# Optimization experiments

Hardware: AMD Instinct MI355X
Metric: run time of the kernel (lower is better)

The kernel has to match this reference:

```python
import jax, jax.numpy as jnp
import numpy as np

D_IN, H, NH = 256, 512, 8
B, T = 8, 1024


def sinusoidal_pe(seq_len, d_model):
    pos = jnp.arange(seq_len, dtype=jnp.float32)[:, None]
    div = jnp.exp(jnp.arange(0, d_model, 2, dtype=jnp.float32) * (-jnp.log(10000.0) / d_model))
    pe = jnp.zeros((seq_len, d_model), jnp.float32)
    pe = pe.at[:, 0::2].set(jnp.sin(pos * div)).at[:, 1::2].set(jnp.cos(pos * div))
    return pe


def layer_norm(x, g, b, eps=1e-5):
    mu = jnp.mean(x, -1, keepdims=True)
    var = jnp.mean((x - mu) ** 2, -1, keepdims=True)
    return (x - mu) * jax.lax.rsqrt(var + eps) * g + b


def lstm_dir(x, wih, whh, bih, bhh):
    # x: [B,T,H]; wih/whh: [4H,H]; gate order i,f,g,o (PyTorch convention)
    Bx = x.shape[0]
    Hh = whh.shape[1]
    xg = jnp.einsum('bth,gh->btg', x, wih) + bih  # precompute input gates [B,T,4H]

    def step(carry, xg_t):
        h, c = carry
        gates = xg_t + h @ whh.T + bhh
        i, f, g, o = jnp.split(gates, 4, axis=-1)
        c = jax.nn.sigmoid(f) * c + jax.nn.sigmoid(i) * jnp.tanh(g)
        h = jax.nn.sigmoid(o) * jnp.tanh(c)
        return (h, c), h

    h0 = jnp.zeros((Bx, Hh), x.dtype)
    _, hs = jax.lax.scan(step, (h0, h0), xg.transpose(1, 0, 2))
    return hs.transpose(1, 0, 2)  # [B,T,H]


def setup_inputs():
    key = jax.random.key(0)
    ks = jax.random.split(key, 30)
    s = 0.02

    def g(k, shape):
        return jax.random.normal(k, shape, jnp.float32) * s

    return {
        'temporal_data': jax.random.normal(ks[0], (B, T, D_IN), jnp.float32),
        'w_in': g(ks[1], (H, D_IN)), 'b_in': jnp.zeros((H,), jnp.float32),
        'wq': g(ks[2], (H, H)), 'bq': jnp.zeros((H,), jnp.float32),
        'wk': g(ks[3], (H, H)), 'bk': jnp.zeros((H,), jnp.float32),
        'wv': g(ks[4], (H, H)), 'bv': jnp.zeros((H,), jnp.float32),
        'wo': g(ks[5], (H, H)), 'bo': jnp.zeros((H,), jnp.float32),
        'g1': jnp.ones((H,), jnp.float32), 'b1': jnp.zeros((H,), jnp.float32),
        'wih_f': g(ks[6], (4 * H, H)), 'whh_f': g(ks[7], (4 * H, H)),
        'bih_f': jnp.zeros((4 * H,), jnp.float32), 'bhh_f': jnp.zeros((4 * H,), jnp.float32),
        'wih_b': g(ks[8], (4 * H, H)), 'whh_b': g(ks[9], (4 * H, H)),
        'bih_b': jnp.zeros((4 * H,), jnp.float32), 'bhh_b': jnp.zeros((4 * H,), jnp.float32),
        'g2': jnp.ones((2 * H,), jnp.float32), 'b2': jnp.zeros((2 * H,), jnp.float32),
        'w_out': g(ks[10], (H, 2 * H)), 'b_out': jnp.zeros((H,), jnp.float32),
    }


def reference(temporal_data, w_in, b_in, wq, bq, wk, bk, wv, bv, wo, bo, g1, b1,
              wih_f, whh_f, bih_f, bhh_f, wih_b, whh_b, bih_b, bhh_b, g2, b2, w_out, b_out):
    x = temporal_data @ w_in.T + b_in                      # [B,T,H]
    Bx, Tx, _ = x.shape
    x = x + sinusoidal_pe(Tx, H)
    residual = x

    hd = H // NH
    q = (x @ wq.T + bq).reshape(Bx, Tx, NH, hd).transpose(0, 2, 1, 3)
    k = (x @ wk.T + bk).reshape(Bx, Tx, NH, hd).transpose(0, 2, 1, 3)
    v = (x @ wv.T + bv).reshape(Bx, Tx, NH, hd).transpose(0, 2, 1, 3)
    scores = jnp.einsum('bhqd,bhkd->bhqk', q, k) * (hd ** -0.5)
    causal = jnp.triu(jnp.ones((Tx, Tx), bool), 1)
    scores = jnp.where(causal, jnp.float32(-1e9), scores)
    attn = jax.nn.softmax(scores, axis=-1)
    o = jnp.einsum('bhqk,bhkd->bhqd', attn, v).transpose(0, 2, 1, 3).reshape(Bx, Tx, H)
    o = o @ wo.T + bo

    x = layer_norm(o + residual, g1, b1)                   # dropout in eval = identity

    h_fwd = lstm_dir(x, wih_f, whh_f, bih_f, bhh_f)
    h_bwd = jnp.flip(lstm_dir(jnp.flip(x, 1), wih_b, whh_b, bih_b, bhh_b), 1)
    lstm_out = jnp.concatenate([h_fwd, h_bwd], axis=-1)    # [B,T,2H]
    lstm_out = layer_norm(lstm_out, g2, b2)

    emb = jnp.mean(lstm_out, axis=1)                       # [B,2H]
    return emb @ w_out.T + b_out                           # [B,H]
```

## Files before the change

### kernel.cpp

```cpp
#include <hip/hip_runtime.h>

typedef unsigned short u16;
typedef unsigned int   u32;
typedef unsigned long long u64;
typedef __attribute__((ext_vector_type(8))) short short8v;
typedef __attribute__((ext_vector_type(4))) float f32x4;
typedef __attribute__((ext_vector_type(4))) unsigned int u32x4;

#define DINL __device__ __forceinline__

DINL u16 f2bf(float f){ union{float f;u32 u;} v{f}; return (u16)((v.u + 0x7fffu + ((v.u>>16)&1u))>>16); }
DINL float bf2f(u16 b){ union{u32 u;float f;} v{(u32)b<<16}; return v.f; }
DINL f32x4 MFMA16(short8v a, short8v b, f32x4 c){ return __builtin_amdgcn_mfma_f32_16x16x32_bf16(a,b,c,0,0,0); }
DINL void gl16(const void* g, void* l){
  __builtin_amdgcn_global_load_lds((const __attribute__((address_space(1))) void*)g,
                                   (__attribute__((address_space(3))) void*)l, 16, 0, 0);
}
DINL float wredd(float v){
#pragma unroll
  for (int m=1;m<64;m<<=1) v += __shfl_xor(v, m);
  return v;
}
DINL float sigm(float x){ return 1.f/(1.f+__expf(-x)); }
DINL float tanh_(float x){ return 2.f/(1.f+__expf(-2.f*x)) - 1.f; }

__global__ __launch_bounds__(256) void zerok(u32* __restrict__ dst){
  size_t i = ((size_t)blockIdx.x*256 + threadIdx.x)*4;
  u32x4 z = {0,0,0,0};
  *(u32x4*)(dst + i) = z;
}

__global__ __launch_bounds__(256) void cvtk(const float* __restrict__ src, u16* __restrict__ dst, int n){
  int i = (blockIdx.x*256 + threadIdx.x)*4;
  float4 v = *(const float4*)(src + i);
  dst[i+0]=f2bf(v.x); dst[i+1]=f2bf(v.y); dst[i+2]=f2bf(v.z); dst[i+3]=f2bf(v.w);
}

template<int EPI>
__global__ __launch_bounds__(256) void gemm128(
    const u16* __restrict__ A, const u16* __restrict__ W,
    const float* __restrict__ bias0, const float* __restrict__ bias1, const float* __restrict__ bias2,
    const u16* __restrict__ resid, u16* __restrict__ out, int M, int N, int K)
{
  __shared__ __align__(16) u16 Al[128*64];
  __shared__ __align__(16) u16 Bl[128*64];
  const int tid = threadIdx.x, lane = tid & 63, w = tid >> 6;
  const int wr = w >> 1, wc = w & 1;
  const int m0 = blockIdx.y * 128, n0 = blockIdx.x * 128;
  f32x4 acc[4][4] = {};
  for (int k0 = 0; k0 < K; k0 += 64) {
#pragma unroll
    for (int j = 0; j < 4; ++j) {
      int idx = (j*4 + w)*64 + lane;
      int r = idx >> 3, c8 = idx & 7;
      gl16(A + (size_t)(m0 + r)*K + k0 + c8*8, (void*)(Al + (size_t)(j*4+w)*512));
      gl16(W + (size_t)(n0 + r)*K + k0 + c8*8, (void*)(Bl + (size_t)(j*4+w)*512));
    }
    __syncthreads();
#pragma unroll
    for (int kk = 0; kk < 2; ++kk) {
      short8v af[4], bf[4];
#pragma unroll
      for (int i = 0; i < 4; ++i)
        af[i] = *(const short8v*)(Al + ((wr*64 + i*16 + (lane&15))*64 + kk*32 + (lane>>4)*8));
#pragma unroll
      for (int i = 0; i < 4; ++i)
        bf[i] = *(const short8v*)(Bl + ((wc*64 + i*16 + (lane&15))*64 + kk*32 + (lane>>4)*8));
#pragma unroll
      for (int mi=0;mi<4;++mi)
#pragma unroll
        for (int ni=0;ni<4;++ni)
          acc[mi][ni] = MFMA16(af[mi], bf[ni], acc[mi][ni]);
    }
    __syncthreads();
  }
#pragma unroll
  for (int mi=0;mi<4;++mi)
#pragma unroll
    for (int ni=0;ni<4;++ni)
#pragma unroll
      for (int r=0;r<4;++r) {
        int m = m0 + wr*64 + mi*16 + (lane>>4)*4 + r;
        int n = n0 + wc*64 + ni*16 + (lane&15);
        float v = acc[mi][ni][r];
        if constexpr (EPI == 0) {
          int t = m & 1023;
          float ang = (float)t * expf((float)(n & ~1) * (-9.210340371976184f/512.f));
          v += bias0[n] + ((n & 1) ? cosf(ang) : sinf(ang));
          out[(size_t)m*512 + n] = f2bf(v);
        } else if constexpr (EPI == 1) {
          int g = n >> 9, n5 = n & 511, hh = n5 >> 6, dh = n5 & 63;
          v += (g==0 ? bias0 : g==1 ? bias1 : bias2)[n5];
          size_t bh = (size_t)((m>>10)*8 + hh);
          u16 val = f2bf(v);
          if (g == 0)      out[(bh*1024 + (m&1023))*64 + dh] = val;
          else if (g == 1) out[4194304 + (bh*1024 + (m&1023))*64 + dh] = val;
          else             out[8388608 + (bh*64 + dh)*1024 + (m&1023)] = val;
        } else {
          v += bias0[n] + bf2f(resid[(size_t)m*512 + n]);
          out[(size_t)m*512 + n] = f2bf(v);
        }
      }
}

__global__ __launch_bounds__(256) void attnk(const u16* __restrict__ qb, const u16* __restrict__ kb,
                                             const u16* __restrict__ vt, u16* __restrict__ attno)
{
  __shared__ __align__(16) u16 P[4][16][72];
  const int tid = threadIdx.x, lane = tid & 63, w = tid >> 6;
  const int bh = blockIdx.x >> 4, qblk = blockIdx.x & 15;
  const int b = bh >> 3, h = bh & 7;
  const float scale = 0.125f;
  short8v qf[2];
  {
    const u16* qbase = qb + ((size_t)bh*1024 + qblk*64 + w*16)*64;
#pragma unroll
    for (int kk=0;kk<2;++kk)
      qf[kk] = *(const short8v*)(qbase + (size_t)(lane&15)*64 + kk*32 + (lane>>4)*8);
  }
  f32x4 o[4] = {};
  float mrun[4], lrun[4];
#pragma unroll
  for (int r=0;r<4;++r){ mrun[r] = -1e30f; lrun[r] = 0.f; }
  for (int kblk = 0; kblk <= qblk; ++kblk) {
    f32x4 s[4] = {};
#pragma unroll
    for (int kk=0;kk<2;++kk)
#pragma unroll
      for (int nt=0;nt<4;++nt) {
        short8v kf = *(const short8v*)(kb + ((size_t)bh*1024 + kblk*64 + nt*16 + (lane&15))*64 + kk*32 + (lane>>4)*8);
        s[nt] = MFMA16(qf[kk], kf, s[nt]);
      }
    float pnew[4][4];
#pragma unroll
    for (int r=0;r<4;++r) {
      int q = qblk*64 + w*16 + (lane>>4)*4 + r;
      float sv[4]; float rowmax = -1e30f;
#pragma unroll
      for (int nt=0;nt<4;++nt) {
        int key = kblk*64 + nt*16 + (lane&15);
        float x = s[nt][r]*scale;
        if (key > q) x = -1e30f;
        sv[nt] = x; rowmax = fmaxf(rowmax, x);
      }
#pragma unroll
      for (int msk=1; msk<16; msk<<=1) rowmax = fmaxf(rowmax, __shfl_xor(rowmax, msk));
      float mnew = fmaxf(mrun[r], rowmax);
      float sf = __expf(mrun[r]-mnew);
      float psum = 0.f;
#pragma unroll
      for (int nt=0;nt<4;++nt){ float p = __expf(sv[nt]-mnew); pnew[nt][r]=p; psum += p; }
#pragma unroll
      for (int msk=1; msk<16; msk<<=1) psum += __shfl_xor(psum, msk);
      lrun[r] = lrun[r]*sf + psum;
      mrun[r] = mnew;
#pragma unroll
      for (int nt=0;nt<4;++nt) o[nt][r] *= sf;
    }
#pragma unroll
    for (int nt=0;nt<4;++nt)
#pragma unroll
      for (int r=0;r<4;++r)
        P[w][(lane>>4)*4+r][nt*16+(lane&15)] = f2bf(pnew[nt][r]);
#pragma unroll
    for (int kk=0;kk<2;++kk) {
      short8v pf = *(const short8v*)&P[w][lane&15][kk*32 + (lane>>4)*8];
#pragma unroll
      for (int nt=0;nt<4;++nt) {
        short8v vf = *(const short8v*)(vt + ((size_t)bh*64 + nt*16 + (lane&15))*1024 + kblk*64 + kk*32 + (lane>>4)*8);
        o[nt] = MFMA16(pf, vf, o[nt]);
      }
    }
  }
#pragma unroll
  for (int nt=0;nt<4;++nt)
#pragma unroll
    for (int r=0;r<4;++r) {
      int q = qblk*64 + w*16 + (lane>>4)*4 + r;
      int dh = nt*16 + (lane&15);
      attno[((size_t)b*1024 + q)*512 + h*64 + dh] = f2bf(o[nt][r] / lrun[r]);
    }
}

__global__ __launch_bounds__(256) void ln1k(const u16* __restrict__ pre, const float* __restrict__ g1,
                                            const float* __restrict__ b1, u16* __restrict__ xl){
  int row = blockIdx.x*4 + (threadIdx.x>>6), lane = threadIdx.x&63;
  short8v xv = *(const short8v*)(pre + (size_t)row*512 + lane*8);
  float v[8], s=0.f, s2=0.f;
#pragma unroll
  for (int e=0;e<8;++e){ v[e]=bf2f((u16)xv[e]); s+=v[e]; s2+=v[e]*v[e]; }
  s = wredd(s); s2 = wredd(s2);
  float mu = s*(1.f/512.f);
  float rs = rsqrtf(s2*(1.f/512.f) - mu*mu + 1e-5f);
  int b = row>>10, t = row&1023;
  short8v ov;
#pragma unroll
  for (int e=0;e<8;++e){ int c=lane*8+e; ov[e]=(short)f2bf((v[e]-mu)*rs*g1[c]+b1[c]); }
  *(short8v*)(xl + ((size_t)t*8 + b)*512 + lane*8) = ov;
}

__global__ __launch_bounds__(256) void lstmk(
    const u16* __restrict__ xl,
    const float* __restrict__ wih_f, const float* __restrict__ whh_f,
    const float* __restrict__ bih_f, const float* __restrict__ bhh_f,
    const float* __restrict__ wih_b, const float* __restrict__ whh_b,
    const float* __restrict__ bih_b, const float* __restrict__ bhh_b,
    u32* __restrict__ ht)
{
  extern __shared__ char smem[];
  u16*  WI  = (u16*)smem;
  u16*  WH  = (u16*)(smem + 65536);
  float* RED = (float*)(smem + 131072);

  const int tid = threadIdx.x, lane = tid&63, w = tid>>6;
  const int d = blockIdx.x >> 5, slice = blockIdx.x & 31, u0 = slice*16;
  const float* WIHg = d ? wih_b : wih_f;
  const float* WHHg = d ? whh_b : whh_f;
  const float* BIH  = d ? bih_b : bih_f;
  const float* BHH  = d ? bhh_b : bhh_f;

  for (int f = tid; f < 4096; f += 256) {
    int nt = f>>10, kc = (f>>6)&15, l = f&63;
    size_t grow = (size_t)(nt*512 + u0 + (l&15));
    int k = kc*32 + (l>>4)*8;
    const float* pi = WIHg + grow*512 + k;
    const float* ph = WHHg + grow*512 + k;
    short8v wa, wb;
#pragma unroll
    for (int e=0;e<8;++e){ wa[e]=(short)f2bf(pi[e]); wb[e]=(short)f2bf(ph[e]); }
    *(short8v*)(WI + (size_t)f*8) = wa;
    *(short8v*)(WH + (size_t)f*8) = wb;
  }
  __syncthreads();

  const bool act = tid < 128;
  const int b_ = tid>>4, u_ = tid&15;
  float c_state = 0.f, bias_c[4];
  if (act)
#pragma unroll
    for (int g=0;g<4;++g) bias_c[g] = BIH[g*512+u0+u_] + BHH[g*512+u0+u_];

  for (int t = 0; t < 1024; ++t) {
    const int te = d ? 1023 - t : t;
    f32x4 acc[4] = {};
    {
      const u16* xb = xl + ((size_t)te*8 + (lane&7))*512;
#pragma unroll
      for (int kk=0;kk<4;++kk) {
        const int kc = w*4 + kk;
        short8v xf = *(const short8v*)(xb + kc*32 + (lane>>4)*8);
#pragma unroll
        for (int nt=0;nt<4;++nt)
          acc[nt] = MFMA16(xf, *(const short8v*)(WI + ((size_t)(nt*16+kc)*64 + lane)*8), acc[nt]);
      }
    }
    if (t > 0) {
      const int tp = d ? 1024 - t : t - 1;
      const u32 tg = (u32)t;
      const u32* pb = ht + ((size_t)(d*1024 + tp)*8 + (lane&7))*512 + (size_t)w*128 + (lane>>4)*8;
      u32x4 q0,q1,q2,q3,q4,q5,q6,q7;
      for (;;) {
        asm volatile(
          "global_load_dwordx4 %0, %8, off sc0 sc1\n\t"
          "global_load_dwordx4 %1, %8, off offset:16 sc0 sc1\n\t"
          "global_load_dwordx4 %2, %8, off offset:128 sc0 sc1\n\t"
          "global_load_dwordx4 %3, %8, off offset:144 sc0 sc1\n\t"
          "global_load_dwordx4 %4, %8, off offset:256 sc0 sc1\n\t"
          "global_load_dwordx4 %5, %8, off offset:272 sc0 sc1\n\t"
          "global_load_dwordx4 %6, %8, off offset:384 sc0 sc1\n\t"
          "global_load_dwordx4 %7, %8, off offset:400 sc0 sc1\n\t"
          "s_waitcnt vmcnt(0)"
          : "=&v"(q0),"=&v"(q1),"=&v"(q2),"=&v"(q3),
            "=&v"(q4),"=&v"(q5),"=&v"(q6),"=&v"(q7)
          : "v"(pb));
        bool ok = true;
#pragma unroll
        for (int e=0;e<4;++e) {
          ok = ok && ((q0[e]&0xffffu)==tg) && ((q1[e]&0xffffu)==tg)
                  && ((q2[e]&0xffffu)==tg) && ((q3[e]&0xffffu)==tg)
                  && ((q4[e]&0xffffu)==tg) && ((q5[e]&0xffffu)==tg)
                  && ((q6[e]&0xffffu)==tg) && ((q7[e]&0xffffu)==tg);
        }
        if (__all(ok)) break;
        __builtin_amdgcn_s_sleep(1);
      }
      const u32x4 qa[8] = {q0,q1,q2,q3,q4,q5,q6,q7};
#pragma unroll
      for (int kk=0;kk<4;++kk) {
        short8v hf;
#pragma unroll
        for (int e=0;e<4;++e) {
          hf[e]   = (short)(qa[2*kk][e]   >> 16);
          hf[4+e] = (short)(qa[2*kk+1][e] >> 16);
        }
        const int kc = w*4 + kk;
#pragma unroll
        for (int nt=0;nt<4;++nt)
          acc[nt] = MFMA16(hf, *(const short8v*)(WH + ((size_t)(nt*16+kc)*64 + lane)*8), acc[nt]);
      }
    }
    float* R = RED + (size_t)(t & 1)*2048;
    if (lane < 32)
#pragma unroll
      for (int nt=0;nt<4;++nt)
        *(f32x4*)(R + ((size_t)(w*4+nt)*32 + lane)*4) = acc[nt];
    __syncthreads();
    if (act) {
      const int lc = u_ + 16*(b_>>2), rg = b_&3;
      float gates[4];
#pragma unroll
      for (int g=0;g<4;++g) {
        float s = 0.f;
#pragma unroll
        for (int wv=0;wv<4;++wv) s += R[((size_t)(wv*4+g)*32 + lc)*4 + rg];
        gates[g] = s + bias_c[g];
      }
      float ig = sigm(gates[0]), fg = sigm(gates[1]), gg = tanh_(gates[2]), og = sigm(gates[3]);
      c_state = fg*c_state + ig*gg;
      u32 word = ((u32)f2bf(og * tanh_(c_state)) << 16) | (u32)(t + 1);
      u32* dst = ht + ((size_t)(d*1024 + te)*8 + b_)*512 + u0 + u_;
      asm volatile("global_store_dword %0, %1, off sc0 sc1" :: "v"(dst), "v"(word) : "memory");
    }
  }
}

__global__ __launch_bounds__(256) void ln2k(const u32* __restrict__ ht, const float* __restrict__ g2,
                                            const float* __restrict__ b2, float* __restrict__ emb){
  __shared__ float accl[4][1024];
  int b = blockIdx.x>>4, chunk = blockIdx.x&15;
  int lane = threadIdx.x&63, w = threadIdx.x>>6;
  for (int i=lane;i<1024;i+=64) accl[w][i]=0.f;
#pragma unroll 1
  for (int i=0;i<16;++i) {
    int t = chunk*64 + w*16 + i;
    const u32* pf = ht + ((size_t)t*8 + b)*512 + lane*8;
    const u32* pb = ht + ((size_t)(1024+t)*8 + b)*512 + lane*8;
    float vf[8], vb[8], s=0.f, s2=0.f;
#pragma unroll
    for (int e=0;e<8;++e){
      vf[e]=bf2f((u16)(pf[e]>>16)); vb[e]=bf2f((u16)(pb[e]>>16));
      s += vf[e]+vb[e]; s2 += vf[e]*vf[e]+vb[e]*vb[e];
    }
    s = wredd(s); s2 = wredd(s2);
    float mu = s*(1.f/1024.f);
    float rs = rsqrtf(s2*(1.f/1024.f) - mu*mu + 1e-5f);
#pragma unroll
    for (int e=0;e<8;++e){
      int c = lane*8+e;
      accl[w][c]     += (vf[e]-mu)*rs*g2[c]     + b2[c];
      accl[w][512+c] += (vb[e]-mu)*rs*g2[512+c] + b2[512+c];
    }
  }
  __syncthreads();
  for (int c = threadIdx.x; c < 1024; c += 256)
    atomicAdd(emb + (size_t)b*1024 + c, accl[0][c]+accl[1][c]+accl[2][c]+accl[3][c]);
}

__global__ __launch_bounds__(256) void fink(const float* __restrict__ emb, const float* __restrict__ w_out,
                                            const float* __restrict__ b_out, float* __restrict__ out){
  int gid = blockIdx.x*256 + threadIdx.x;
  int n = gid>>3, b = gid&7;
  const float* e = emb + (size_t)b*1024;
  const float* wr = w_out + (size_t)n*1024;
  float s = 0.f;
  for (int k=0;k<1024;k+=4) {
    float4 ev = *(const float4*)(e+k);
    float4 wv = *(const float4*)(wr+k);
    s += ev.x*wv.x + ev.y*wv.y + ev.z*wv.z + ev.w*wv.w;
  }
  out[(size_t)b*512 + n] = b_out[n] + s*(1.f/1024.f);
}

#define OFF_EMB   0u
#define OFF_A0    36864u
#define OFF_WIN   4231168u
#define OFF_WQKV  4493312u
#define OFF_WO    6066176u
#define OFF_X0B   6590464u
#define OFF_QB    14979072u
#define OFF_PRE   14979072u
#define OFF_XL    23367680u
#define OFF_ATT   40144896u
#define OFF_HT    48533504u

extern "C" void kernel_launch(void* const* d_in, const int* in_sizes, int n_in,
                              void* d_out, int out_size, void* d_ws, size_t ws_size,
                              hipStream_t stream) {
  const float* temporal = (const float*)d_in[0];
  const float* w_in = (const float*)d_in[1];  const float* b_in = (const float*)d_in[2];
  const float* wq = (const float*)d_in[3];    const float* bq = (const float*)d_in[4];
  const float* wk = (const float*)d_in[5];    const float* bk = (const float*)d_in[6];
  const float* wv = (const float*)d_in[7];    const float* bv = (const float*)d_in[8];
  const float* wo = (const float*)d_in[9];    const float* bo = (const float*)d_in[10];
  const float* g1 = (const float*)d_in[11];   const float* b1 = (const float*)d_in[12];
  const float* wih_f = (const float*)d_in[13]; const float* whh_f = (const float*)d_in[14];
  const float* bih_f = (const float*)d_in[15]; const float* bhh_f = (const float*)d_in[16];
  const float* wih_b = (const float*)d_in[17]; const float* whh_b = (const float*)d_in[18];
  const float* bih_b = (const float*)d_in[19]; const float* bhh_b = (const float*)d_in[20];
  const float* g2 = (const float*)d_in[21];   const float* b2 = (const float*)d_in[22];
  const float* w_out = (const float*)d_in[23]; const float* b_out = (const float*)d_in[24];

  char* ws = (char*)d_ws;
  float* EMB = (float*)(ws + OFF_EMB);
  u16* A0   = (u16*)(ws + OFF_A0);
  u16* WIN  = (u16*)(ws + OFF_WIN);
  u16* WQKV = (u16*)(ws + OFF_WQKV);
  u16* WOb  = (u16*)(ws + OFF_WO);
  u16* X0B  = (u16*)(ws + OFF_X0B);
  u16* QB   = (u16*)(ws + OFF_QB);
  u16* PRE  = (u16*)(ws + OFF_PRE);
  u16* XL   = (u16*)(ws + OFF_XL);
  u16* ATT  = (u16*)(ws + OFF_ATT);
  u32* HT   = (u32*)(ws + OFF_HT);

  (void)hipFuncSetAttribute((const void*)lstmk, hipFuncAttributeMaxDynamicSharedMemorySize, 147456);

  zerok<<<8192,256,0,stream>>>(HT);
  zerok<<<8,   256,0,stream>>>((u32*)(ws + OFF_EMB));

  cvtk<<<2048,256,0,stream>>>(temporal, A0, 2097152);
  cvtk<<<128, 256,0,stream>>>(w_in, WIN, 131072);
  cvtk<<<256, 256,0,stream>>>(wq, WQKV,           262144);
  cvtk<<<256, 256,0,stream>>>(wk, WQKV + 262144,  262144);
  cvtk<<<256, 256,0,stream>>>(wv, WQKV + 524288,  262144);
  cvtk<<<256, 256,0,stream>>>(wo, WOb, 262144);

  gemm128<0><<<dim3(4,64), 256, 0, stream>>>(A0, WIN, b_in, nullptr, nullptr, nullptr, X0B, 8192, 512, 256);
  gemm128<1><<<dim3(12,64),256, 0, stream>>>(X0B, WQKV, bq, bk, bv, nullptr, QB, 8192, 1536, 512);
  attnk<<<1024,256,0,stream>>>(QB, QB + 4194304, QB + 8388608, ATT);
  gemm128<3><<<dim3(4,64), 256, 0, stream>>>(ATT, WOb, bo, nullptr, nullptr, X0B, PRE, 8192, 512, 512);
  ln1k<<<2048,256,0,stream>>>(PRE, g1, b1, XL);
  lstmk<<<64,256,147456,stream>>>(XL, wih_f, whh_f, bih_f, bhh_f, wih_b, whh_b, bih_b, bhh_b, HT);
  ln2k<<<128,256,0,stream>>>(HT, g2, b2, EMB);
  fink<<<16,256,0,stream>>>(EMB, w_out, b_out, (float*)d_out);
}
```

Before: 3.569 ms.

## Use small double-buffered exchange buffer for LSTM hidden-state sync and separate bf16 output

The LSTM's cross-block hidden-state exchange moves from a full [2,1024,8,512] u32 tagged array to a tiny double-buffered [2 dirs,2 slots,8,512] buffer, and the bf16 hidden outputs are written to a separate compact array read by the LayerNorm kernel. This drops the large zeroing of the tagged array and keeps the polled exchange data small enough to stay resident in cache. The cost is an extra store per step. Reusing the two slots depends on the step tag, so a block that runs far ahead could overwrite a slot before slower blocks have read it.

```diff
diff --git a/kernel.cpp b/kernel.cpp
--- a/kernel.cpp
+++ b/kernel.cpp
@@ -205,7 +205,7 @@
     const float* __restrict__ bih_f, const float* __restrict__ bhh_f,
     const float* __restrict__ wih_b, const float* __restrict__ whh_b,
     const float* __restrict__ bih_b, const float* __restrict__ bhh_b,
-    u32* __restrict__ ht)
+    u32* __restrict__ hx, u16* __restrict__ hs)
 {
   extern __shared__ char smem[];
   u16*  WI  = (u16*)smem;
@@ -255,9 +255,8 @@
       }
     }
     if (t > 0) {
-      const int tp = d ? 1024 - t : t - 1;
       const u32 tg = (u32)t;
-      const u32* pb = ht + ((size_t)(d*1024 + tp)*8 + (lane&7))*512 + (size_t)w*128 + (lane>>4)*8;
+      const u32* pb = hx + ((size_t)d*2 + ((t-1)&1))*4096 + (size_t)(lane&7)*512 + (size_t)w*128 + (lane>>4)*8;
       u32x4 q0,q1,q2,q3,q4,q5,q6,q7;
       for (;;) {
         asm volatile(
@@ -317,14 +316,16 @@
       }
       float ig = sigm(gates[0]), fg = sigm(gates[1]), gg = tanh_(gates[2]), og = sigm(gates[3]);
       c_state = fg*c_state + ig*gg;
-      u32 word = ((u32)f2bf(og * tanh_(c_state)) << 16) | (u32)(t + 1);
-      u32* dst = ht + ((size_t)(d*1024 + te)*8 + b_)*512 + u0 + u_;
+      u16 hv = f2bf(og * tanh_(c_state));
+      hs[((size_t)(d*1024 + te)*8 + b_)*512 + u0 + u_] = hv;
+      u32 word = ((u32)hv << 16) | (u32)(t + 1);
+      u32* dst = hx + ((size_t)d*2 + (t&1))*4096 + (size_t)b_*512 + u0 + u_;
       asm volatile("global_store_dword %0, %1, off sc0 sc1" :: "v"(dst), "v"(word) : "memory");
     }
   }
 }
 
-__global__ __launch_bounds__(256) void ln2k(const u32* __restrict__ ht, const float* __restrict__ g2,
+__global__ __launch_bounds__(256) void ln2k(const u16* __restrict__ hs, const float* __restrict__ g2,
                                             const float* __restrict__ b2, float* __restrict__ emb){
   __shared__ float accl[4][1024];
   int b = blockIdx.x>>4, chunk = blockIdx.x&15;
@@ -333,14 +334,12 @@
 #pragma unroll 1
   for (int i=0;i<16;++i) {
     int t = chunk*64 + w*16 + i;
-    const u32* pf = ht + ((size_t)t*8 + b)*512 + lane*8;
-    const u32* pb = ht + ((size_t)(1024+t)*8 + b)*512 + lane*8;
+    short8v xf = *(const short8v*)(hs + ((size_t)t*8 + b)*512 + lane*8);
+    short8v xb = *(const short8v*)(hs + ((size_t)(1024+t)*8 + b)*512 + lane*8);
     float vf[8], vb[8], s=0.f, s2=0.f;
 #pragma unroll
-    for (int e=0;e<8;++e){
-      vf[e]=bf2f((u16)(pf[e]>>16)); vb[e]=bf2f((u16)(pb[e]>>16));
-      s += vf[e]+vb[e]; s2 += vf[e]*vf[e]+vb[e]*vb[e];
-    }
+    for (int e=0;e<8;++e){ vf[e]=bf2f((u16)xf[e]); vb[e]=bf2f((u16)xb[e]);
+                           s += vf[e]+vb[e]; s2 += vf[e]*vf[e]+vb[e]*vb[e]; }
     s = wredd(s); s2 = wredd(s2);
     float mu = s*(1.f/1024.f);
     float rs = rsqrtf(s2*(1.f/1024.f) - mu*mu + 1e-5f);
@@ -372,16 +371,17 @@
 }
 
 #define OFF_EMB   0u
-#define OFF_A0    36864u
-#define OFF_WIN   4231168u
-#define OFF_WQKV  4493312u
-#define OFF_WO    6066176u
-#define OFF_X0B   6590464u
-#define OFF_QB    14979072u
-#define OFF_PRE   14979072u
-#define OFF_XL    23367680u
-#define OFF_ATT   40144896u
-#define OFF_HT    48533504u
+#define OFF_HX    32768u
+#define OFF_A0    98304u
+#define OFF_WIN   4292608u
+#define OFF_WQKV  4554752u
+#define OFF_WO    6127616u
+#define OFF_X0B   6651904u
+#define OFF_QB    15040512u
+#define OFF_PRE   15040512u
+#define OFF_XL    23429120u
+#define OFF_ATT   40206336u
+#define OFF_HS    48594944u
 
 extern "C" void kernel_launch(void* const* d_in, const int* in_sizes, int n_in,
                               void* d_out, int out_size, void* d_ws, size_t ws_size,
@@ -402,6 +402,7 @@
 
   char* ws = (char*)d_ws;
   float* EMB = (float*)(ws + OFF_EMB);
+  u32* HX   = (u32*)(ws + OFF_HX);
   u16* A0   = (u16*)(ws + OFF_A0);
   u16* WIN  = (u16*)(ws + OFF_WIN);
   u16* WQKV = (u16*)(ws + OFF_WQKV);
@@ -411,12 +412,11 @@
   u16* PRE  = (u16*)(ws + OFF_PRE);
   u16* XL   = (u16*)(ws + OFF_XL);
   u16* ATT  = (u16*)(ws + OFF_ATT);
-  u32* HT   = (u32*)(ws + OFF_HT);
+  u16* HS   = (u16*)(ws + OFF_HS);
 
   (void)hipFuncSetAttribute((const void*)lstmk, hipFuncAttributeMaxDynamicSharedMemorySize, 147456);
 
-  zerok<<<8192,256,0,stream>>>(HT);
-  zerok<<<8,   256,0,stream>>>((u32*)(ws + OFF_EMB));
+  zerok<<<24,256,0,stream>>>((u32*)(ws + OFF_EMB));
 
   cvtk<<<2048,256,0,stream>>>(temporal, A0, 2097152);
   cvtk<<<128, 256,0,stream>>>(w_in, WIN, 131072);
@@ -430,7 +430,7 @@
   attnk<<<1024,256,0,stream>>>(QB, QB + 4194304, QB + 8388608, ATT);
   gemm128<3><<<dim3(4,64), 256, 0, stream>>>(ATT, WOb, bo, nullptr, nullptr, X0B, PRE, 8192, 512, 512);
   ln1k<<<2048,256,0,stream>>>(PRE, g1, b1, XL);
-  lstmk<<<64,256,147456,stream>>>(XL, wih_f, whh_f, bih_f, bhh_f, wih_b, whh_b, bih_b, bhh_b, HT);
-  ln2k<<<128,256,0,stream>>>(HT, g2, b2, EMB);
+  lstmk<<<64,256,147456,stream>>>(XL, wih_f, whh_f, bih_f, bhh_f, wih_b, whh_b, bih_b, bhh_b, HX, HS);
+  ln2k<<<128,256,0,stream>>>(HS, g2, b2, EMB);
   fink<<<16,256,0,stream>>>(EMB, w_out, b_out, (float*)d_out);
 }
```

Result: no change. 3.578 ms (+0.2%).
